# Optimization experiments

Hardware: AMD Instinct MI355X
Metric: run time of the kernel (lower is better)

Reference implementation:

```python
import jax, jax.numpy as jnp
import numpy as np

NUM_ORI = 4
VM_R, VM_RG = 10.0, 15.0
B_INH, G_INH = 1.5, 1.0
VM_W, VM_W2 = 0.1, 0.4
VM_WG, VM_W2G = 0.2, 0.4
BORDER_K = 11   # int(10*1.1)=11, already odd
GROUP_K = 23    # int(15*1.5)=22 -> +1 to make odd


def create_von_mises(size, r0, theta0, centered, w, w2):
    x = np.arange(size) - size / 2
    y = -(np.arange(size) - size / 2)
    X, Y = np.meshgrid(x, y)
    if centered:
        X = X + r0 * np.cos(theta0)
        Y = Y + r0 * np.sin(theta0)
    r = np.sqrt(X ** 2 + Y ** 2)
    th = np.arctan2(Y, X)
    # np.i0 == scipy.special.iv(0, .) for real args (I0 is even)
    return np.exp(r0 * w * np.cos(th - theta0)) / np.i0(w2 * (r - r0))


def make_filters():
    borders, groups = [], []
    for ori in np.arange(0.0, 180.0, 180.0 / NUM_ORI):
        a = ori * np.pi / 180.0
        b = (ori + 180.0) * np.pi / 180.0
        borders.append(create_von_mises(BORDER_K, VM_R, a, True, VM_W, VM_W2))
        borders.append(create_von_mises(BORDER_K, VM_R, b, True, VM_W, VM_W2))
        g1 = create_von_mises(GROUP_K, VM_RG, a, False, VM_W, VM_W2)
        g2 = create_von_mises(GROUP_K, VM_RG, b, False, VM_WG, VM_W2G)
        groups += [g1, g1, g2, g2]
    # only border filters are normalized to [-1, 1] in the original code
    borders = [f / (f.max() / 2.0) - 1.0 for f in borders]
    Wb = np.stack(borders)[:, None].astype(np.float32)   # [2*O, 1, 11, 11]
    Wg = np.stack(groups)[:, None].astype(np.float32)    # [4*O, 1, 23, 23]
    return jnp.asarray(Wb), jnp.asarray(Wg)


def setup_inputs() -> dict:
    key = jax.random.key(0)
    inp = jax.random.uniform(key, (4, 2, 512, 512), dtype=jnp.float32)
    Wb, Wg = make_filters()
    return {"inp": inp, "W_border": Wb, "W_group": Wg}


def _conv(x, w, pad, groups):
    return jax.lax.conv_general_dilated(
        x, w, (1, 1), [(pad, pad), (pad, pad)],
        dimension_numbers=("NCHW", "OIHW", "NCHW"),
        feature_group_count=groups)


def _spike(v):
    # LIF with tau_mem=0.01, zero initial v_mem, single step: alpha=exp(-1/tau)~0,
    # so v_mem = input; spike when v_mem >= threshold (1.0).
    return (v >= 1.0).astype(v.dtype)


def reference(inp, W_border, W_group):
    B, _, H, W = inp.shape
    pad_b = (BORDER_K - 1) // 2
    pad_g = (GROUP_K - 1) // 2
    # border ownership: conv each polarity with the 8 von-Mises filters + LIF
    pos = _spike(_conv(inp[:, 0:1], W_border, pad_b, 1))  # [B, 2*O, H, W]
    neg = _spike(_conv(inp[:, 1:2], W_border, pad_b, 1))
    vmap_ = inp.sum(1)[:, None]                           # [B, 1, H, W]
    pe, po = pos[:, 0::2], pos[:, 1::2]   # even=ori, odd=opposite ori
    ne, no = neg[:, 0::2], neg[:, 1::2]
    b13 = _spike(vmap_ * (pe - no * B_INH)) + _spike(vmap_ * (ne - po * B_INH))
    b24 = _spike(vmap_ * (po - ne * B_INH)) + _spike(vmap_ * (no - pe * B_INH))
    # winner-take-all over orientations
    diff = b13 - b24                                      # [B, O, H, W]
    tp = jnp.abs(diff)
    wta = jax.lax.stop_gradient(
        (tp == tp.max(axis=1, keepdims=True)).astype(inp.dtype))
    b1p = _spike(wta * diff)
    b1n = _spike(-(wta * diff))
    # channel order is ori-major: [t1_o, t2_o, t3_o, t4_o] per orientation
    border = jnp.stack(
        [b1p * b13, b1p * b24 * G_INH, b1n * b24, b1n * b13 * G_INH],
        axis=2).reshape(B, 4 * NUM_ORI, H, W)
    g = _spike(_conv(border, W_group, pad_g, 4 * NUM_ORI))
    g = g.reshape(B, NUM_ORI, 4, H, W)
    return (_spike(g[:, :, 0] - g[:, :, 1])
            + _spike(g[:, :, 2] - g[:, :, 3])).sum(1)     # [B, H, W]
```

## Files before the change

kernel.cpp:

```cpp
#include <hip/hip_runtime.h>

#define HH 512
#define WW 512
#define NB 4

#define K1 11
#define PAD1 5
#define T1X 32
#define T1Y 16
#define IN1X 42
#define IN1Y 26
#define S1 44

__device__ __forceinline__ unsigned conv8_pass2(const float* __restrict__ sm,
                                                const float* __restrict__ Wb,
                                                int py, int px)
{
    float acc[8][2];
    #pragma unroll
    for (int c = 0; c < 8; c++) { acc[c][0] = 0.f; acc[c][1] = 0.f; }

    #pragma unroll 1
    for (int ky = 0; ky < K1; ky++) {
        const float2* rp = (const float2*)&sm[(py + ky) * S1 + px];
        float a[12];
        #pragma unroll
        for (int r = 0; r < 6; r++) *(float2*)&a[2 * r] = rp[r];
        #pragma unroll
        for (int c = 0; c < 8; c++) {
            #pragma unroll
            for (int kx = 0; kx < K1; kx++) {
                const float wv = Wb[c * 121 + ky * 11 + kx];
                acc[c][0] = fmaf(a[kx],     wv, acc[c][0]);
                acc[c][1] = fmaf(a[kx + 1], wv, acc[c][1]);
            }
        }
    }
    unsigned bits = 0;
    #pragma unroll
    for (int c = 0; c < 8; c++) {
        bits |= (acc[c][0] >= 1.f ? 1u : 0u) << (c * 2);
        bits |= (acc[c][1] >= 1.f ? 1u : 0u) << (c * 2 + 1);
    }
    return bits;
}

__global__ __launch_bounds__(256, 8) void stage1_kernel(
    const float* __restrict__ inp, const float* __restrict__ Wb,
    unsigned char* __restrict__ border)
{
    __shared__ __align__(16) float s0[IN1Y * S1];
    __shared__ __align__(16) float s1[IN1Y * S1];

    const int b   = blockIdx.z;
    const int tx0 = blockIdx.x * T1X;
    const int ty0 = blockIdx.y * T1Y;
    const float* in0 = inp + ((size_t)b * 2 + 0) * (HH * WW);
    const float* in1 = inp + ((size_t)b * 2 + 1) * (HH * WW);

    for (int i = threadIdx.x; i < IN1Y * IN1X; i += 256) {
        int iy = i / IN1X, ix = i - iy * IN1X;
        int gy = ty0 + iy - PAD1, gx = tx0 + ix - PAD1;
        bool ok = (gy >= 0) & (gy < HH) & (gx >= 0) & (gx < WW);
        int idx = gy * WW + gx;
        s0[iy * S1 + ix] = ok ? in0[idx] : 0.f;
        s1[iy * S1 + ix] = ok ? in1[idx] : 0.f;
    }
    __syncthreads();

    const int lx = threadIdx.x & 15;
    const int ly = threadIdx.x >> 4;
    const int px = lx * 2;
    const int py = ly;

    const unsigned bitP = conv8_pass2(s0, Wb, py, px);
    const unsigned bitN = conv8_pass2(s1, Wb, py, px);

    const int gy = ty0 + py;
    const int gxbase = tx0 + px;

    float vm[2];
    #pragma unroll
    for (int p = 0; p < 2; p++)
        vm[p] = s0[(py + PAD1) * S1 + px + PAD1 + p]
              + s1[(py + PAD1) * S1 + px + PAD1 + p];

    float b13[4][2], b24[4][2];
    #pragma unroll
    for (int o = 0; o < 4; o++) {
        #pragma unroll
        for (int p = 0; p < 2; p++) {
            float pe = (float)((bitP >> (4 * o + p))     & 1u);
            float po = (float)((bitP >> (4 * o + 2 + p)) & 1u);
            float ne = (float)((bitN >> (4 * o + p))     & 1u);
            float no = (float)((bitN >> (4 * o + 2 + p)) & 1u);
            float sa = (vm[p] * (pe - 1.5f * no) >= 1.f) ? 1.f : 0.f;
            float sb = (vm[p] * (ne - 1.5f * po) >= 1.f) ? 1.f : 0.f;
            b13[o][p] = sa + sb;
            float sc = (vm[p] * (po - 1.5f * ne) >= 1.f) ? 1.f : 0.f;
            float sd = (vm[p] * (no - 1.5f * pe) >= 1.f) ? 1.f : 0.f;
            b24[o][p] = sc + sd;
        }
    }
    float mxp[2];
    #pragma unroll
    for (int p = 0; p < 2; p++) {
        float m = 0.f;
        #pragma unroll
        for (int o = 0; o < 4; o++) m = fmaxf(m, fabsf(b13[o][p] - b24[o][p]));
        mxp[p] = m;
    }
    #pragma unroll
    for (int o = 0; o < 4; o++) {
        unsigned short w0 = 0, w1 = 0, w2 = 0, w3 = 0;
        #pragma unroll
        for (int p = 0; p < 2; p++) {
            float d   = b13[o][p] - b24[o][p];
            float wta = (fabsf(d) == mxp[p]) ? 1.f : 0.f;
            float b1p = (wta * d >= 1.f)    ? 1.f : 0.f;
            float b1n = (-(wta * d) >= 1.f) ? 1.f : 0.f;
            w0 |= (unsigned short)(unsigned char)(b1p * b13[o][p]) << (8 * p);
            w1 |= (unsigned short)(unsigned char)(b1p * b24[o][p]) << (8 * p);
            w2 |= (unsigned short)(unsigned char)(b1n * b24[o][p]) << (8 * p);
            w3 |= (unsigned short)(unsigned char)(b1n * b13[o][p]) << (8 * p);
        }
        size_t base = (((size_t)b * 16 + 4 * o) * HH + gy) * WW + gxbase;
        *(unsigned short*)&border[base]                       = w0;
        *(unsigned short*)&border[base + (size_t)HH * WW]     = w1;
        *(unsigned short*)&border[base + (size_t)2 * HH * WW] = w2;
        *(unsigned short*)&border[base + (size_t)3 * HH * WW] = w3;
    }
}

#define K2 23
#define PAD2 11
#define T2X 32
#define T2Y 128
#define SROW 18
#define R2 150

__device__ __forceinline__ float ubyte_f(unsigned dw, int byi) {
    return (float)((dw >> (8 * byi)) & 0xffu);
}

__global__ __launch_bounds__(256, 4) void stage2_kernel(
    const unsigned char* __restrict__ border, const float* __restrict__ Wg,
    unsigned char* __restrict__ gsp)
{
    __shared__ unsigned tile[R2 * SROW];

    const int z   = blockIdx.z;
    const int b   = z >> 4;
    const int c   = z & 15;
    const int tx0 = blockIdx.x * T2X;
    const int ty0 = blockIdx.y * T2Y;
    const unsigned char* bp = border + ((size_t)b * 16 + c) * (HH * WW);

    for (int i = threadIdx.x; i < R2 * 16; i += 256) {
        int iy = i >> 4, cc = i & 15;
        int gy  = ty0 - PAD2 + iy;
        int gx0 = tx0 - 12 + 4 * cc;
        unsigned u = 0;
        if (((unsigned)gy < HH) & ((unsigned)gx0 < WW))
            u = *(const unsigned*)(bp + (size_t)gy * WW + gx0);
        tile[iy * SROW + cc] = u;
    }
    __syncthreads();

    const int lx = threadIdx.x & 3;
    const int ly = threadIdx.x >> 2;
    const int px = lx * 8;
    const int py = ly * 2;

    float acc[2][8];
    #pragma unroll
    for (int dy = 0; dy < 2; dy++)
        #pragma unroll
        for (int p = 0; p < 8; p++) acc[dy][p] = 0.f;

    const float* wc = Wg + c * (K2 * K2);

    #pragma unroll 1
    for (int kyb = 0; kyb < 7; kyb++) {
        const int b0 = kyb * 3;
        #pragma unroll
        for (int r = 0; r < 4; r++) {
            const int trow = py + b0 + r;
            unsigned d[8];
            const uint2* tp2 = (const uint2*)&tile[trow * SROW + 2 * lx];
            #pragma unroll
            for (int r2 = 0; r2 < 4; r2++) { uint2 v = tp2[r2]; d[2*r2] = v.x; d[2*r2+1] = v.y; }
            float a[31];
            #pragma unroll
            for (int j = 1; j <= 30; j++) a[j] = ubyte_f(d[j >> 2], j & 3);
            #pragma unroll
            for (int jk = 0; jk < 3; jk++) {
                const int dy = r - jk;
                if (dy >= 0 && dy < 2) {
                    #pragma unroll
                    for (int kx = 0; kx < 23; kx++) {
                        const float wv = wc[(b0 + jk) * 23 + kx];
                        #pragma unroll
                        for (int p = 0; p < 8; p++)
                            acc[dy][p] = fmaf(a[p + kx + 1], wv, acc[dy][p]);
                    }
                }
            }
        }
    }
    {
        const int b0 = 21;
        #pragma unroll
        for (int r = 0; r < 3; r++) {
            const int trow = py + b0 + r;
            unsigned d[8];
            const uint2* tp2 = (const uint2*)&tile[trow * SROW + 2 * lx];
            #pragma unroll
            for (int r2 = 0; r2 < 4; r2++) { uint2 v = tp2[r2]; d[2*r2] = v.x; d[2*r2+1] = v.y; }
            float a[31];
            #pragma unroll
            for (int j = 1; j <= 30; j++) a[j] = ubyte_f(d[j >> 2], j & 3);
            #pragma unroll
            for (int jk = 0; jk < 2; jk++) {
                const int dy = r - jk;
                if (dy >= 0 && dy < 2) {
                    #pragma unroll
                    for (int kx = 0; kx < 23; kx++) {
                        const float wv = wc[(b0 + jk) * 23 + kx];
                        #pragma unroll
                        for (int p = 0; p < 8; p++)
                            acc[dy][p] = fmaf(a[p + kx + 1], wv, acc[dy][p]);
                    }
                }
            }
        }
    }

    const int ox = tx0 + px;
    unsigned char* gp = gsp + ((size_t)b * 16 + c) * (HH * WW);
    #pragma unroll
    for (int dy = 0; dy < 2; dy++) {
        const int oy = ty0 + py + dy;
        unsigned lo = 0, hi = 0;
        #pragma unroll
        for (int p = 0; p < 4; p++) lo |= (acc[dy][p]     >= 1.f ? 1u : 0u) << (8 * p);
        #pragma unroll
        for (int p = 0; p < 4; p++) hi |= (acc[dy][p + 4] >= 1.f ? 1u : 0u) << (8 * p);
        uint2 v; v.x = lo; v.y = hi;
        *(uint2*)&gp[(size_t)oy * WW + ox] = v;
    }
}

__global__ __launch_bounds__(256) void combine_kernel(
    const unsigned char* __restrict__ gsp, float* __restrict__ out)
{
    const int idx = blockIdx.x * 256 + threadIdx.x;
    const int b = idx >> 16;
    const int r = idx & 65535;
    const unsigned* g = (const unsigned*)gsp;
    const int pb = b * 16;
    unsigned s = 0;
    #pragma unroll
    for (int o = 0; o < 4; o++) {
        unsigned g0 = g[(size_t)(pb + 4 * o + 0) * 65536 + r];
        unsigned g1 = g[(size_t)(pb + 4 * o + 1) * 65536 + r];
        unsigned g2 = g[(size_t)(pb + 4 * o + 2) * 65536 + r];
        unsigned g3 = g[(size_t)(pb + 4 * o + 3) * 65536 + r];
        s += ((g0 & ~g1) & 0x01010101u) + ((g2 & ~g3) & 0x01010101u);
    }
    float4 f;
    f.x = (float)(s & 255u);
    f.y = (float)((s >> 8) & 255u);
    f.z = (float)((s >> 16) & 255u);
    f.w = (float)(s >> 24);
    ((float4*)out)[idx] = f;
}

extern "C" void kernel_launch(void* const* d_in, const int* in_sizes, int n_in,
                              void* d_out, int out_size, void* d_ws, size_t ws_size,
                              hipStream_t stream)
{
    const float* inp = (const float*)d_in[0];
    const float* Wb  = (const float*)d_in[1];
    const float* Wg  = (const float*)d_in[2];
    unsigned char* border = (unsigned char*)d_ws;
    unsigned char* gsp    = border + (size_t)NB * 16 * HH * WW;
    float* out = (float*)d_out;

    dim3 blk(256);
    dim3 g1(WW / T1X, HH / T1Y, NB);
    stage1_kernel<<<g1, blk, 0, stream>>>(inp, Wb, border);
    dim3 g2(WW / T2X, HH / T2Y, NB * 16);
    stage2_kernel<<<g2, blk, 0, stream>>>(border, Wg, gsp);
    dim3 g3((NB * HH * WW / 4) / 256);
    combine_kernel<<<g3, blk, 0, stream>>>(gsp, out);
}
```

Measured before the change: 289.3 us.

## Pair group channels in stage2, store fp16 tile, fuse AND-NOT into stage2

Each stage2 block now processes both channels of a pair (g0/g1 or g2/g3) one after the other and computes the g_a & ~g_b term in registers. It writes 8 term planes instead of 16 spike planes, which halves intermediate writes and simplifies the combine kernel to a plain sum. The shared tile now holds bytes pre-converted to fp16, so the inner loop does cheap half-to-float extraction instead of byte unpacking. The cost is a larger shared tile, a serial dependency between the two channels inside each block, and half as many blocks.

```diff
diff --git a/kernel.cpp b/kernel.cpp
--- a/kernel.cpp
+++ b/kernel.cpp
@@ -1,4 +1,5 @@
 #include <hip/hip_runtime.h>
+#include <hip/hip_fp16.h>
 
 #define HH 512
 #define WW 512
@@ -136,138 +137,151 @@
 #define PAD2 11
 #define T2X 32
 #define T2Y 128
-#define SROW 18
+#define F16ROW 28
 #define R2 150
-
-__device__ __forceinline__ float ubyte_f(unsigned dw, int byi) {
-    return (float)((dw >> (8 * byi)) & 0xffu);
-}
 
 __global__ __launch_bounds__(256, 4) void stage2_kernel(
     const unsigned char* __restrict__ border, const float* __restrict__ Wg,
-    unsigned char* __restrict__ gsp)
-{
-    __shared__ unsigned tile[R2 * SROW];
+    unsigned char* __restrict__ termp)
+{
+    __shared__ __align__(16) unsigned tile[R2 * F16ROW];
 
     const int z   = blockIdx.z;
-    const int b   = z >> 4;
-    const int c   = z & 15;
+    const int b   = z >> 3;
+    const int pr  = z & 7;
     const int tx0 = blockIdx.x * T2X;
     const int ty0 = blockIdx.y * T2Y;
-    const unsigned char* bp = border + ((size_t)b * 16 + c) * (HH * WW);
-
-    for (int i = threadIdx.x; i < R2 * 16; i += 256) {
-        int iy = i >> 4, cc = i & 15;
-        int gy  = ty0 - PAD2 + iy;
-        int gx0 = tx0 - 12 + 4 * cc;
-        unsigned u = 0;
-        if (((unsigned)gy < HH) & ((unsigned)gx0 < WW))
-            u = *(const unsigned*)(bp + (size_t)gy * WW + gx0);
-        tile[iy * SROW + cc] = u;
-    }
-    __syncthreads();
 
     const int lx = threadIdx.x & 3;
     const int ly = threadIdx.x >> 2;
     const int px = lx * 8;
     const int py = ly * 2;
 
-    float acc[2][8];
-    #pragma unroll
-    for (int dy = 0; dy < 2; dy++)
-        #pragma unroll
-        for (int p = 0; p < 8; p++) acc[dy][p] = 0.f;
-
-    const float* wc = Wg + c * (K2 * K2);
+    unsigned sprev = 0, term = 0;
 
     #pragma unroll 1
-    for (int kyb = 0; kyb < 7; kyb++) {
-        const int b0 = kyb * 3;
-        #pragma unroll
-        for (int r = 0; r < 4; r++) {
-            const int trow = py + b0 + r;
-            unsigned d[8];
-            const uint2* tp2 = (const uint2*)&tile[trow * SROW + 2 * lx];
-            #pragma unroll
-            for (int r2 = 0; r2 < 4; r2++) { uint2 v = tp2[r2]; d[2*r2] = v.x; d[2*r2+1] = v.y; }
-            float a[31];
-            #pragma unroll
-            for (int j = 1; j <= 30; j++) a[j] = ubyte_f(d[j >> 2], j & 3);
-            #pragma unroll
-            for (int jk = 0; jk < 3; jk++) {
-                const int dy = r - jk;
-                if (dy >= 0 && dy < 2) {
-                    #pragma unroll
-                    for (int kx = 0; kx < 23; kx++) {
-                        const float wv = wc[(b0 + jk) * 23 + kx];
+    for (int h = 0; h < 2; h++) {
+        const int c = 2 * pr + h;
+        const unsigned char* bp = border + ((size_t)b * 16 + c) * (HH * WW);
+        if (h) __syncthreads();
+
+        for (int i = threadIdx.x; i < R2 * 14; i += 256) {
+            int iy = i / 14, cc = i - iy * 14;
+            int gy  = ty0 - PAD2 + iy;
+            int gx0 = tx0 - 12 + 4 * cc;
+            unsigned u = 0;
+            if (((unsigned)gy < HH) & ((unsigned)gx0 < WW))
+                u = *(const unsigned*)(bp + (size_t)gy * WW + gx0);
+            __half2 lo2 = __floats2half2_rn((float)(u & 255u), (float)((u >> 8) & 255u));
+            __half2 hi2 = __floats2half2_rn((float)((u >> 16) & 255u), (float)(u >> 24));
+            unsigned* dst = &tile[iy * F16ROW + 2 * cc];
+            dst[0] = *(unsigned*)&lo2;
+            dst[1] = *(unsigned*)&hi2;
+        }
+        __syncthreads();
+
+        float acc[2][8];
+        #pragma unroll
+        for (int dy = 0; dy < 2; dy++)
+            #pragma unroll
+            for (int p = 0; p < 8; p++) acc[dy][p] = 0.f;
+
+        const float* wc = Wg + c * (K2 * K2);
+
+        #pragma unroll 1
+        for (int kyb = 0; kyb < 7; kyb++) {
+            const int b0 = kyb * 3;
+            #pragma unroll
+            for (int r = 0; r < 4; r++) {
+                const int trow = py + b0 + r;
+                unsigned d[16];
+                const uint4* tp4 = (const uint4*)&tile[trow * F16ROW + 4 * lx];
+                #pragma unroll
+                for (int rr = 0; rr < 4; rr++) *(uint4*)&d[4 * rr] = tp4[rr];
+                #pragma unroll
+                for (int jk = 0; jk < 3; jk++) {
+                    const int dy = r - jk;
+                    if (dy >= 0 && dy < 2) {
                         #pragma unroll
-                        for (int p = 0; p < 8; p++)
-                            acc[dy][p] = fmaf(a[p + kx + 1], wv, acc[dy][p]);
+                        for (int kx = 0; kx < 23; kx++) {
+                            const float wv = wc[(b0 + jk) * 23 + kx];
+                            #pragma unroll
+                            for (int p = 0; p < 8; p++) {
+                                const int e = p + kx + 1;
+                                __half2 h2 = *(__half2*)&d[e >> 1];
+                                float xv = (e & 1) ? __high2float(h2) : __low2float(h2);
+                                acc[dy][p] = fmaf(xv, wv, acc[dy][p]);
+                            }
+                        }
                     }
                 }
             }
         }
-    }
-    {
-        const int b0 = 21;
-        #pragma unroll
-        for (int r = 0; r < 3; r++) {
-            const int trow = py + b0 + r;
-            unsigned d[8];
-            const uint2* tp2 = (const uint2*)&tile[trow * SROW + 2 * lx];
-            #pragma unroll
-            for (int r2 = 0; r2 < 4; r2++) { uint2 v = tp2[r2]; d[2*r2] = v.x; d[2*r2+1] = v.y; }
-            float a[31];
-            #pragma unroll
-            for (int j = 1; j <= 30; j++) a[j] = ubyte_f(d[j >> 2], j & 3);
-            #pragma unroll
-            for (int jk = 0; jk < 2; jk++) {
-                const int dy = r - jk;
-                if (dy >= 0 && dy < 2) {
-                    #pragma unroll
-                    for (int kx = 0; kx < 23; kx++) {
-                        const float wv = wc[(b0 + jk) * 23 + kx];
+        {
+            const int b0 = 21;
+            #pragma unroll
+            for (int r = 0; r < 3; r++) {
+                const int trow = py + b0 + r;
+                unsigned d[16];
+                const uint4* tp4 = (const uint4*)&tile[trow * F16ROW + 4 * lx];
+                #pragma unroll
+                for (int rr = 0; rr < 4; rr++) *(uint4*)&d[4 * rr] = tp4[rr];
+                #pragma unroll
+                for (int jk = 0; jk < 2; jk++) {
+                    const int dy = r - jk;
+                    if (dy >= 0 && dy < 2) {
                         #pragma unroll
-                        for (int p = 0; p < 8; p++)
-                            acc[dy][p] = fmaf(a[p + kx + 1], wv, acc[dy][p]);
+                        for (int kx = 0; kx < 23; kx++) {
+                            const float wv = wc[(b0 + jk) * 23 + kx];
+                            #pragma unroll
+                            for (int p = 0; p < 8; p++) {
+                                const int e = p + kx + 1;
+                                __half2 h2 = *(__half2*)&d[e >> 1];
+                                float xv = (e & 1) ? __high2float(h2) : __low2float(h2);
+                                acc[dy][p] = fmaf(xv, wv, acc[dy][p]);
+                            }
+                        }
                     }
                 }
             }
         }
+
+        unsigned s = 0;
+        #pragma unroll
+        for (int dy = 0; dy < 2; dy++)
+            #pragma unroll
+            for (int p = 0; p < 8; p++)
+                s |= (acc[dy][p] >= 1.f ? 1u : 0u) << (8 * dy + p);
+        if (h == 0) sprev = s;
+        else        term  = sprev & ~s;
     }
 
     const int ox = tx0 + px;
-    unsigned char* gp = gsp + ((size_t)b * 16 + c) * (HH * WW);
+    unsigned char* gp = termp + ((size_t)b * 8 + pr) * (HH * WW);
     #pragma unroll
     for (int dy = 0; dy < 2; dy++) {
-        const int oy = ty0 + py + dy;
         unsigned lo = 0, hi = 0;
         #pragma unroll
-        for (int p = 0; p < 4; p++) lo |= (acc[dy][p]     >= 1.f ? 1u : 0u) << (8 * p);
-        #pragma unroll
-        for (int p = 0; p < 4; p++) hi |= (acc[dy][p + 4] >= 1.f ? 1u : 0u) << (8 * p);
+        for (int p = 0; p < 4; p++) {
+            lo |= ((term >> (8 * dy + p))     & 1u) << (8 * p);
+            hi |= ((term >> (8 * dy + 4 + p)) & 1u) << (8 * p);
+        }
         uint2 v; v.x = lo; v.y = hi;
-        *(uint2*)&gp[(size_t)oy * WW + ox] = v;
+        *(uint2*)&gp[(size_t)(ty0 + py + dy) * WW + ox] = v;
     }
 }
 
 __global__ __launch_bounds__(256) void combine_kernel(
-    const unsigned char* __restrict__ gsp, float* __restrict__ out)
+    const unsigned char* __restrict__ termp, float* __restrict__ out)
 {
     const int idx = blockIdx.x * 256 + threadIdx.x;
     const int b = idx >> 16;
     const int r = idx & 65535;
-    const unsigned* g = (const unsigned*)gsp;
-    const int pb = b * 16;
+    const unsigned* g = (const unsigned*)termp;
     unsigned s = 0;
     #pragma unroll
-    for (int o = 0; o < 4; o++) {
-        unsigned g0 = g[(size_t)(pb + 4 * o + 0) * 65536 + r];
-        unsigned g1 = g[(size_t)(pb + 4 * o + 1) * 65536 + r];
-        unsigned g2 = g[(size_t)(pb + 4 * o + 2) * 65536 + r];
-        unsigned g3 = g[(size_t)(pb + 4 * o + 3) * 65536 + r];
-        s += ((g0 & ~g1) & 0x01010101u) + ((g2 & ~g3) & 0x01010101u);
-    }
+    for (int p = 0; p < 8; p++)
+        s += g[(size_t)(b * 8 + p) * 65536 + r];
     float4 f;
     f.x = (float)(s & 255u);
     f.y = (float)((s >> 8) & 255u);
@@ -284,14 +298,14 @@
     const float* Wb  = (const float*)d_in[1];
     const float* Wg  = (const float*)d_in[2];
     unsigned char* border = (unsigned char*)d_ws;
-    unsigned char* gsp    = border + (size_t)NB * 16 * HH * WW;
+    unsigned char* termp  = border + (size_t)NB * 16 * HH * WW;
     float* out = (float*)d_out;
 
     dim3 blk(256);
     dim3 g1(WW / T1X, HH / T1Y, NB);
     stage1_kernel<<<g1, blk, 0, stream>>>(inp, Wb, border);
-    dim3 g2(WW / T2X, HH / T2Y, NB * 16);
-    stage2_kernel<<<g2, blk, 0, stream>>>(border, Wg, gsp);
+    dim3 g2(WW / T2X, HH / T2Y, NB * 8);
+    stage2_kernel<<<g2, blk, 0, stream>>>(border, Wg, termp);
     dim3 g3((NB * HH * WW / 4) / 256);
-    combine_kernel<<<g3, blk, 0, stream>>>(gsp, out);
-}
+    combine_kernel<<<g3, blk, 0, stream>>>(termp, out);
+}
```

After: 315.6 us. 9.1% more time.
